# Kernel tuning notes

Hardware: AMD Instinct MI355X
Metric: run time of the kernel (lower is better)

## Reference

```python
import jax, jax.numpy as jnp
import numpy as np

OBS_LEN, K, B, H, MID, NC, CIN = 12, 20, 2048, 128, 256, 2, 3

def setup_inputs() -> dict:
    key = jax.random.key(0)
    ks = jax.random.split(key, 12)
    w = lambda k, s: 0.1 * jax.random.normal(k, s, dtype=jnp.float32)
    return {
        'obs_traj_rel': jax.random.normal(ks[0], (OBS_LEN, B, CIN), dtype=jnp.float32),
        'pred_lstm_hidden': jax.random.normal(ks[1], (K, B, H), dtype=jnp.float32),
        'map_w0': w(ks[2], (H, MID)), 'map_b0': jnp.zeros((MID,), jnp.float32),
        'map_w1': w(ks[3], (MID, H)), 'map_b1': jnp.zeros((H,), jnp.float32),
        'w_ih': w(ks[4], (4 * H, NC)), 'w_hh': w(ks[5], (4 * H, H)),
        'b_ih': jnp.zeros((4 * H,), jnp.float32), 'b_hh': jnp.zeros((4 * H,), jnp.float32),
        'out_w': w(ks[6], (H, NC)), 'out_b': jnp.zeros((NC,), jnp.float32),
    }

def _hard_sigmoid(x):
    # torch F.hardsigmoid: clip(x/6 + 0.5, 0, 1)
    return jnp.clip(x / 6.0 + 0.5, 0.0, 1.0)

def reference(obs_traj_rel, pred_lstm_hidden, map_w0, map_b0, map_w1, map_b1,
              w_ih, w_hh, b_ih, b_hh, out_w, out_b):
    n_coord = out_w.shape[1]
    hdim = w_hh.shape[1]
    # mapping MLP on initial hidden state: [K, B, H]
    h = jax.nn.leaky_relu(pred_lstm_hidden @ map_w0 + map_b0, negative_slope=0.01)
    h = h @ map_w1 + map_b1
    c = jnp.zeros_like(h)
    # step i uses obs[i-1] (obs[0] at i=0), sliced to first n_coord channels
    inputs = jnp.concatenate([obs_traj_rel[:1], obs_traj_rel[:-1]], axis=0)[:, :, :n_coord]  # [T, B, nc]
    bias = b_ih + b_hh

    def step(carry, x_t):
        h, c = carry  # each [K, B, H]
        # x_t [B, nc] broadcast over samples K (same gates contribution for all K)
        gx = x_t @ w_ih.T  # [B, 4H]
        gates = gx[None, :, :] + h @ w_hh.T + bias  # [K, B, 4H]
        i, f, g, o = jnp.split(gates, 4, axis=-1)
        i = _hard_sigmoid(i); f = _hard_sigmoid(f)
        g = jnp.clip(g, -1.0, 1.0); o = _hard_sigmoid(o)
        c_new = f * c + i * g
        h_new = o * jnp.clip(c_new, -1.0, 1.0)
        out = h_new @ out_w + out_b  # [K, B, nc]
        return (h_new, c_new), out

    _, outs = jax.lax.scan(step, (h, c), inputs)
    return outs  # [obs_len, K, B, n_coord]
```

## Files before the change

### kernel.cpp

```cpp
#include <hip/hip_runtime.h>
#include <stdint.h>

#define OBS_LEN 12
#define KS 20
#define BB 2048
#define HD 128
#define MIDD 256
#define NCQ 2

using f32x4  = __attribute__((ext_vector_type(4))) float;
using bf16x8 = __attribute__((ext_vector_type(8))) short;

static __device__ __forceinline__ short f2bf(float f){
  return __builtin_bit_cast(short, (__bf16)f);
}
static __device__ __forceinline__ uint32_t pack2(float a, float b){
  return (uint32_t)(uint16_t)f2bf(a) | ((uint32_t)(uint16_t)f2bf(b) << 16);
}
static __device__ __forceinline__ float hsig(float x){
  return fminf(fmaxf(fmaf(x, 0.16666666666666666f, 0.5f), 0.f), 1.f);
}
static __device__ __forceinline__ float clip1(float x){
  return fminf(fmaxf(x, -1.f), 1.f);
}
static __device__ __forceinline__ f32x4 mm(bf16x8 a, bf16x8 b, f32x4 c){
  return __builtin_amdgcn_mfma_f32_16x16x32_bf16(a, b, c, 0, 0, 0);
}
static __device__ __forceinline__ bf16x8 ldh(const uint16_t* buf, int row, int q, int p){
  return *reinterpret_cast<const bf16x8*>(&buf[(row*HD + q*32 + p*8) ^ ((row&7)*8)]);
}
static __device__ __forceinline__ bf16x8 lda(const uint16_t* buf, int row, int q, int p){
  return *reinterpret_cast<const bf16x8*>(&buf[(row*MIDD + q*32 + p*8) ^ ((row&7)*8)]);
}

__global__ __launch_bounds__(512, 2)
void CRMF_35296041239144_kernel(
    const float* __restrict__ obs,  const float* __restrict__ pred,
    const float* __restrict__ mw0,  const float* __restrict__ mb0,
    const float* __restrict__ mw1,  const float* __restrict__ mb1,
    const float* __restrict__ wih,  const float* __restrict__ whh,
    const float* __restrict__ bih,  const float* __restrict__ bhh,
    const float* __restrict__ oww,  const float* __restrict__ obb,
    float* __restrict__ outp)
{
  __shared__ __align__(16) uint16_t hbuf[32*HD];
  __shared__ __align__(16) uint16_t abuf[32*MIDD];
  __shared__ __align__(16) uint16_t ofrag[4*64*8];
  __shared__ float2 xbuf[OBS_LEN][32];

  const int tid = threadIdx.x;
  const int w   = tid >> 6;
  const int l   = tid & 63;
  const int p   = (tid >> 4) & 3;
  const int ln  = tid & 15;
  const int wofs = w * 16;
  const bool w7 = (w == 7);

  const int b     = blockIdx.x;
  const int b0    = (b & 63) * 32;
  const int kslot = b >> 6;

  if (tid < OBS_LEN*32){
    int t = tid >> 5, cc = tid & 31;
    int st = t ? (t-1) : 0;
    const float* pp = obs + ((size_t)st*BB + b0 + cc)*3;
    xbuf[t][cc] = make_float2(pp[0], pp[1]);
  }
  if (w == 0){
    #pragma unroll
    for (int q=0; q<4; ++q){
      bf16x8 wf;
      #pragma unroll
      for (int j=0; j<8; ++j){
        int k = q*32 + p*8 + j;
        wf[j] = (ln < NCQ) ? f2bf(oww[k*NCQ + ln]) : (short)0;
      }
      *reinterpret_cast<bf16x8*>(&ofrag[(q*64 + l)*8]) = wf;
    }
  }
  const float obv = (ln < NCQ) ? obb[ln] : 0.f;

  bf16x8 wfrag[4][4];
  float wihA[4], wihB[4], biasv[4];
  #pragma unroll
  for (int gate=0; gate<4; ++gate){
    int col = gate*128 + wofs + ln;
    wihA[gate]  = wih[col*2];
    wihB[gate]  = wih[col*2+1];
    biasv[gate] = bih[col] + bhh[col];
    #pragma unroll
    for (int q=0; q<4; ++q){
      const float* s = whh + col*HD + q*32 + p*8;
      float4 f0 = *reinterpret_cast<const float4*>(s);
      float4 f1 = *reinterpret_cast<const float4*>(s+4);
      bf16x8 wf;
      wf[0]=f2bf(f0.x); wf[1]=f2bf(f0.y); wf[2]=f2bf(f0.z); wf[3]=f2bf(f0.w);
      wf[4]=f2bf(f1.x); wf[5]=f2bf(f1.y); wf[6]=f2bf(f1.z); wf[7]=f2bf(f1.w);
      wfrag[gate][q] = wf;
    }
  }

  #pragma unroll 1
  for (int c=0; c<5; ++c){
    const int kk = kslot*5 + c;

    __syncthreads();
    {
      const float* src = pred + ((size_t)(kk*BB + b0))*HD;
      #pragma unroll
      for (int it=0; it<2; ++it){
        int u = tid + it*512;
        int row = u >> 5, c4 = (u & 31)*4;
        float4 v = *reinterpret_cast<const float4*>(src + row*HD + c4);
        int e = (row*HD + c4) ^ ((row&7)*8);
        *reinterpret_cast<uint32_t*>(&hbuf[e])   = pack2(v.x, v.y);
        *reinterpret_cast<uint32_t*>(&hbuf[e+2]) = pack2(v.z, v.w);
      }
    }
    __syncthreads();

    {
      f32x4 acc1[2][2];
      #pragma unroll
      for (int ct=0; ct<2; ++ct){
        float mb = mb0[w*32 + ct*16 + ln];
        f32x4 v = {mb,mb,mb,mb};
        acc1[0][ct]=v; acc1[1][ct]=v;
      }
      #pragma unroll
      for (int q=0; q<4; ++q){
        bf16x8 af0 = ldh(hbuf, ln, q, p), af1 = ldh(hbuf, 16+ln, q, p);
        #pragma unroll
        for (int ct=0; ct<2; ++ct){
          bf16x8 wf;
          #pragma unroll
          for (int j=0; j<8; ++j)
            wf[j] = f2bf(mw0[(q*32+p*8+j)*MIDD + (w*32 + ct*16 + ln)]);
          acc1[0][ct] = mm(af0, wf, acc1[0][ct]);
          acc1[1][ct] = mm(af1, wf, acc1[1][ct]);
        }
      }
      #pragma unroll
      for (int rt=0; rt<2; ++rt)
      #pragma unroll
      for (int ct=0; ct<2; ++ct)
      #pragma unroll
      for (int r=0; r<4; ++r){
        float v = acc1[rt][ct][r];
        v = (v>0.f)? v : 0.01f*v;
        int row = rt*16 + p*4 + r;
        abuf[(row*MIDD + w*32 + ct*16 + ln) ^ ((row&7)*8)] = (uint16_t)f2bf(v);
      }
    }
    __syncthreads();

    float c_[2][4];
    {
      f32x4 acc2[2];
      float mb = mb1[wofs + ln];
      f32x4 v = {mb,mb,mb,mb};
      acc2[0]=v; acc2[1]=v;
      #pragma unroll
      for (int q=0; q<8; ++q){
        bf16x8 af0 = lda(abuf, ln, q, p), af1 = lda(abuf, 16+ln, q, p);
        bf16x8 wf;
        #pragma unroll
        for (int j=0; j<8; ++j)
          wf[j] = f2bf(mw1[(q*32+p*8+j)*HD + wofs + ln]);
        acc2[0] = mm(af0, wf, acc2[0]);
        acc2[1] = mm(af1, wf, acc2[1]);
      }
      #pragma unroll
      for (int rt=0; rt<2; ++rt)
      #pragma unroll
      for (int r=0; r<4; ++r){
        int row = rt*16 + p*4 + r;
        hbuf[(row*HD + wofs + ln) ^ ((row&7)*8)] = (uint16_t)f2bf(acc2[rt][r]);
        c_[rt][r] = 0.f;
      }
    }
    __syncthreads();

    #pragma unroll 1
    for (int t=0; t<OBS_LEN; ++t){
      f32x4 acc[2][4];
      #pragma unroll
      for (int rt=0; rt<2; ++rt){
        #pragma unroll
        for (int r=0; r<4; ++r){
          float2 xv = xbuf[t][rt*16 + p*4 + r];
          #pragma unroll
          for (int gate=0; gate<4; ++gate)
            acc[rt][gate][r] = fmaf(xv.x, wihA[gate], fmaf(xv.y, wihB[gate], biasv[gate]));
        }
      }
      f32x4 a8[2];
      if (w7 && t>0){ f32x4 v={obv,obv,obv,obv}; a8[0]=v; a8[1]=v; }
      #pragma unroll
      for (int q=0; q<4; ++q){
        bf16x8 af0 = ldh(hbuf, ln, q, p), af1 = ldh(hbuf, 16+ln, q, p);
        #pragma unroll
        for (int gate=0; gate<4; ++gate){
          acc[0][gate] = mm(af0, wfrag[gate][q], acc[0][gate]);
          acc[1][gate] = mm(af1, wfrag[gate][q], acc[1][gate]);
        }
        if (w7 && t>0){
          bf16x8 of = *reinterpret_cast<const bf16x8*>(&ofrag[(q*64 + l)*8]);
          a8[0] = mm(af0, of, a8[0]);
          a8[1] = mm(af1, of, a8[1]);
        }
      }
      if (w7 && t>0 && ln<NCQ){
        #pragma unroll
        for (int rt=0; rt<2; ++rt)
        #pragma unroll
        for (int r=0; r<4; ++r){
          int cell = rt*16 + p*4 + r;
          outp[(((size_t)(t-1)*KS + kk)*BB + b0 + cell)*NCQ + ln] = a8[rt][r];
        }
      }
      __syncthreads();
      #pragma unroll
      for (int rt=0; rt<2; ++rt)
      #pragma unroll
      for (int r=0; r<4; ++r){
        float iv = hsig(acc[rt][0][r]);
        float fv = hsig(acc[rt][1][r]);
        float gv = clip1(acc[rt][2][r]);
        float ov = hsig(acc[rt][3][r]);
        float cv = fmaf(fv, c_[rt][r], iv*gv);
        c_[rt][r] = cv;
        int row = rt*16 + p*4 + r;
        hbuf[(row*HD + wofs + ln) ^ ((row&7)*8)] = (uint16_t)f2bf(ov * clip1(cv));
      }
      __syncthreads();
    }

    if (w7){
      f32x4 o0 = {obv,obv,obv,obv}, o1 = o0;
      #pragma unroll
      for (int q=0; q<4; ++q){
        bf16x8 af0 = ldh(hbuf, ln, q, p), af1 = ldh(hbuf, 16+ln, q, p);
        bf16x8 of = *reinterpret_cast<const bf16x8*>(&ofrag[(q*64 + l)*8]);
        o0 = mm(af0, of, o0);
        o1 = mm(af1, of, o1);
      }
      if (ln < NCQ){
        #pragma unroll
        for (int r=0; r<4; ++r){
          outp[(((size_t)11*KS + kk)*BB + b0 +      (p*4+r))*NCQ + ln] = o0[r];
          outp[(((size_t)11*KS + kk)*BB + b0 + 16 + (p*4+r))*NCQ + ln] = o1[r];
        }
      }
    }
  }
}

extern "C" void kernel_launch(void* const* d_in, const int* in_sizes, int n_in,
                              void* d_out, int out_size, void* d_ws, size_t ws_size,
                              hipStream_t stream) {
  (void)in_sizes; (void)n_in; (void)d_ws; (void)ws_size; (void)out_size;
  CRMF_35296041239144_kernel<<<dim3(256), dim3(512), 0, stream>>>(
      (const float*)d_in[0], (const float*)d_in[1], (const float*)d_in[2],
      (const float*)d_in[3], (const float*)d_in[4], (const float*)d_in[5],
      (const float*)d_in[6], (const float*)d_in[7], (const float*)d_in[8],
      (const float*)d_in[9], (const float*)d_in[10], (const float*)d_in[11],
      (float*)d_out);
}
```

Measured before the change: 171.2 us.

## Split K across more blocks, double-buffer hidden state, stage output stores

The grid doubles to 512 blocks. Each block now handles 3 or 2 interleaved sample chunks instead of 5, which shortens the per-block serial path and fills more of the GPU. The LSTM hidden state is double-buffered in LDS, which removes one __syncthreads per timestep. Per-step output writes from a single wave are staged in LDS and flushed with coalesced stores once per chunk. The cost is uneven work across blocks (3 chunks versus 2) and extra shared memory, which may limit co-residency.

```diff
diff --git a/kernel.cpp b/kernel.cpp
--- a/kernel.cpp
+++ b/kernel.cpp
@@ -43,10 +43,11 @@
     const float* __restrict__ oww,  const float* __restrict__ obb,
     float* __restrict__ outp)
 {
-  __shared__ __align__(16) uint16_t hbuf[32*HD];
+  __shared__ __align__(16) uint16_t hbuf[2][32*HD];
   __shared__ __align__(16) uint16_t abuf[32*MIDD];
   __shared__ __align__(16) uint16_t ofrag[4*64*8];
   __shared__ float2 xbuf[OBS_LEN][32];
+  __shared__ float  ostage[OBS_LEN][64];
 
   const int tid = threadIdx.x;
   const int w   = tid >> 6;
@@ -56,9 +57,9 @@
   const int wofs = w * 16;
   const bool w7 = (w == 7);
 
-  const int b     = blockIdx.x;
-  const int b0    = (b & 63) * 32;
-  const int kslot = b >> 6;
+  const int b   = blockIdx.x;
+  const int b0  = (b & 63) * 32;
+  const int nch = (b < 256) ? 3 : 2;
 
   if (tid < OBS_LEN*32){
     int t = tid >> 5, cc = tid & 31;
@@ -101,8 +102,8 @@
   }
 
   #pragma unroll 1
-  for (int c=0; c<5; ++c){
-    const int kk = kslot*5 + c;
+  for (int i=0; i<nch; ++i){
+    const int kk = (b >> 6) + 8*i;
 
     __syncthreads();
     {
@@ -113,8 +114,8 @@
         int row = u >> 5, c4 = (u & 31)*4;
         float4 v = *reinterpret_cast<const float4*>(src + row*HD + c4);
         int e = (row*HD + c4) ^ ((row&7)*8);
-        *reinterpret_cast<uint32_t*>(&hbuf[e])   = pack2(v.x, v.y);
-        *reinterpret_cast<uint32_t*>(&hbuf[e+2]) = pack2(v.z, v.w);
+        *reinterpret_cast<uint32_t*>(&hbuf[0][e])   = pack2(v.x, v.y);
+        *reinterpret_cast<uint32_t*>(&hbuf[0][e+2]) = pack2(v.z, v.w);
       }
     }
     __syncthreads();
@@ -129,7 +130,7 @@
       }
       #pragma unroll
       for (int q=0; q<4; ++q){
-        bf16x8 af0 = ldh(hbuf, ln, q, p), af1 = ldh(hbuf, 16+ln, q, p);
+        bf16x8 af0 = ldh(hbuf[0], ln, q, p), af1 = ldh(hbuf[0], 16+ln, q, p);
         #pragma unroll
         for (int ct=0; ct<2; ++ct){
           bf16x8 wf;
@@ -175,7 +176,7 @@
       #pragma unroll
       for (int r=0; r<4; ++r){
         int row = rt*16 + p*4 + r;
-        hbuf[(row*HD + wofs + ln) ^ ((row&7)*8)] = (uint16_t)f2bf(acc2[rt][r]);
+        hbuf[0][(row*HD + wofs + ln) ^ ((row&7)*8)] = (uint16_t)f2bf(acc2[rt][r]);
         c_[rt][r] = 0.f;
       }
     }
@@ -183,6 +184,7 @@
 
     #pragma unroll 1
     for (int t=0; t<OBS_LEN; ++t){
+      const int cur = t & 1, nxt = cur ^ 1;
       f32x4 acc[2][4];
       #pragma unroll
       for (int rt=0; rt<2; ++rt){
@@ -198,7 +200,7 @@
       if (w7 && t>0){ f32x4 v={obv,obv,obv,obv}; a8[0]=v; a8[1]=v; }
       #pragma unroll
       for (int q=0; q<4; ++q){
-        bf16x8 af0 = ldh(hbuf, ln, q, p), af1 = ldh(hbuf, 16+ln, q, p);
+        bf16x8 af0 = ldh(hbuf[cur], ln, q, p), af1 = ldh(hbuf[cur], 16+ln, q, p);
         #pragma unroll
         for (int gate=0; gate<4; ++gate){
           acc[0][gate] = mm(af0, wfrag[gate][q], acc[0][gate]);
@@ -214,12 +216,9 @@
         #pragma unroll
         for (int rt=0; rt<2; ++rt)
         #pragma unroll
-        for (int r=0; r<4; ++r){
-          int cell = rt*16 + p*4 + r;
-          outp[(((size_t)(t-1)*KS + kk)*BB + b0 + cell)*NCQ + ln] = a8[rt][r];
-        }
-      }
-      __syncthreads();
+        for (int r=0; r<4; ++r)
+          ostage[t-1][(rt*16 + p*4 + r)*NCQ + ln] = a8[rt][r];
+      }
       #pragma unroll
       for (int rt=0; rt<2; ++rt)
       #pragma unroll
@@ -231,7 +230,7 @@
         float cv = fmaf(fv, c_[rt][r], iv*gv);
         c_[rt][r] = cv;
         int row = rt*16 + p*4 + r;
-        hbuf[(row*HD + wofs + ln) ^ ((row&7)*8)] = (uint16_t)f2bf(ov * clip1(cv));
+        hbuf[nxt][(row*HD + wofs + ln) ^ ((row&7)*8)] = (uint16_t)f2bf(ov * clip1(cv));
       }
       __syncthreads();
     }
@@ -240,7 +239,7 @@
       f32x4 o0 = {obv,obv,obv,obv}, o1 = o0;
       #pragma unroll
       for (int q=0; q<4; ++q){
-        bf16x8 af0 = ldh(hbuf, ln, q, p), af1 = ldh(hbuf, 16+ln, q, p);
+        bf16x8 af0 = ldh(hbuf[0], ln, q, p), af1 = ldh(hbuf[0], 16+ln, q, p);
         bf16x8 of = *reinterpret_cast<const bf16x8*>(&ofrag[(q*64 + l)*8]);
         o0 = mm(af0, of, o0);
         o1 = mm(af1, of, o1);
@@ -248,10 +247,16 @@
       if (ln < NCQ){
         #pragma unroll
         for (int r=0; r<4; ++r){
-          outp[(((size_t)11*KS + kk)*BB + b0 +      (p*4+r))*NCQ + ln] = o0[r];
-          outp[(((size_t)11*KS + kk)*BB + b0 + 16 + (p*4+r))*NCQ + ln] = o1[r];
-        }
-      }
+          ostage[11][(     p*4 + r)*NCQ + ln] = o0[r];
+          ostage[11][(16 + p*4 + r)*NCQ + ln] = o1[r];
+        }
+      }
+    }
+    __syncthreads();
+
+    for (int u = tid; u < OBS_LEN*64; u += 512){
+      int t = u >> 6, e = u & 63;
+      outp[((size_t)(t*KS + kk)*BB + b0)*NCQ + e] = ostage[t][e];
     }
   }
 }
@@ -260,7 +265,7 @@
                               void* d_out, int out_size, void* d_ws, size_t ws_size,
                               hipStream_t stream) {
   (void)in_sizes; (void)n_in; (void)d_ws; (void)ws_size; (void)out_size;
-  CRMF_35296041239144_kernel<<<dim3(256), dim3(512), 0, stream>>>(
+  CRMF_35296041239144_kernel<<<dim3(512), dim3(512), 0, stream>>>(
       (const float*)d_in[0], (const float*)d_in[1], (const float*)d_in[2],
       (const float*)d_in[3], (const float*)d_in[4], (const float*)d_in[5],
       (const float*)d_in[6], (const float*)d_in[7], (const float*)d_in[8],
```

After: 213.0 us. 24.4% more time.

## Interleave two K-samples per block, double-buffer hidden state, prepack bf16 weights

Applied to the files above, without the earlier changes.

Each block now runs two sample slices (kk pairs) at once through the mapping MLP and LSTM recurrence. This doubles the independent MFMA chains per wave, which hides MFMA latency and halves the number of barrier-separated steps. The hidden state is double-buffered in shared memory, so one __syncthreads per timestep replaces two. A separate prep kernel converts and pre-swizzles W_hh, the mapping weights and the output weights into bf16 fragment layout in the workspace, replacing per-element strided fp32 loads and conversions. The cost is roughly double the LDS footprint and more registers, which may cut occupancy below the two blocks per CU the launch bounds request, plus one extra kernel launch.

```diff
diff --git a/kernel.cpp b/kernel.cpp
--- a/kernel.cpp
+++ b/kernel.cpp
@@ -8,6 +8,12 @@
 #define MIDD 256
 #define NCQ 2
 
+#define WSW_OFF  0
+#define WSM0_OFF 65536
+#define WSM1_OFF 98304
+#define WSO_OFF  131072
+#define WS_ELEMS 133120
+
 using f32x4  = __attribute__((ext_vector_type(4))) float;
 using bf16x8 = __attribute__((ext_vector_type(8))) short;
 
@@ -33,6 +39,299 @@
   return *reinterpret_cast<const bf16x8*>(&buf[(row*MIDD + q*32 + p*8) ^ ((row&7)*8)]);
 }
 
+__global__ void CRMF_prep_kernel(const float* __restrict__ mw0,
+                                 const float* __restrict__ mw1,
+                                 const float* __restrict__ whh,
+                                 const float* __restrict__ oww,
+                                 uint16_t* __restrict__ ws)
+{
+  int f = blockIdx.x*256 + threadIdx.x;
+  if (f >= 16640) return;
+  bf16x8 out;
+  int dst;
+  if (f < 8192){
+    int l=f&63, q=(f>>6)&3, gate=(f>>8)&3, w=f>>10;
+    int col = gate*128 + w*16 + (l&15);
+    const float* s = whh + col*HD + q*32 + ((l>>4)&3)*8;
+    #pragma unroll
+    for (int j=0;j<8;++j) out[j] = f2bf(s[j]);
+    dst = WSW_OFF + f*8;
+  } else if (f < 12288){
+    int ff=f-8192; int l=ff&63, q=(ff>>6)&3, ct=(ff>>8)&1, w=ff>>9;
+    int col = w*32 + ct*16 + (l&15);
+    int r0 = q*32 + ((l>>4)&3)*8;
+    #pragma unroll
+    for (int j=0;j<8;++j) out[j] = f2bf(mw0[(r0+j)*MIDD + col]);
+    dst = WSM0_OFF + ff*8;
+  } else if (f < 16384){
+    int ff=f-12288; int l=ff&63, q=(ff>>6)&7, w=ff>>9;
+    int col = w*16 + (l&15);
+    int r0 = q*32 + ((l>>4)&3)*8;
+    #pragma unroll
+    for (int j=0;j<8;++j) out[j] = f2bf(mw1[(r0+j)*HD + col]);
+    dst = WSM1_OFF + ff*8;
+  } else {
+    int ff=f-16384; int l=ff&63, q=ff>>6;
+    int ln=l&15; int r0 = q*32 + ((l>>4)&3)*8;
+    #pragma unroll
+    for (int j=0;j<8;++j) out[j] = (ln<NCQ) ? f2bf(oww[(r0+j)*NCQ + ln]) : (short)0;
+    dst = WSO_OFF + ff*8;
+  }
+  *reinterpret_cast<bf16x8*>(&ws[dst]) = out;
+}
+
+template<bool FWS, bool HASB>
+static __device__ __forceinline__ void run_pair(
+    int kkA, int kkB, int b0,
+    const float* __restrict__ pred,
+    const float* __restrict__ mb0, const float* __restrict__ mb1,
+    const float* __restrict__ mw0, const float* __restrict__ mw1,
+    const uint16_t* __restrict__ ws,
+    const bf16x8 (&wfrag)[4][4],
+    const float (&wihA)[4], const float (&wihB)[4], const float (&biasv)[4],
+    const uint16_t* ofrag, float obv,
+    uint16_t (*hA)[32*HD], uint16_t (*hB)[32*HD],
+    uint16_t* abA, uint16_t* abB,
+    const float2 (&xbuf)[OBS_LEN][32],
+    float* __restrict__ outp,
+    int tid, int w, int l, int p, int ln, int wofs, bool w7)
+{
+  __syncthreads();
+
+  {
+    const float* srcA = pred + ((size_t)(kkA*BB + b0))*HD;
+    #pragma unroll
+    for (int it=0; it<2; ++it){
+      int u = tid + it*512;
+      int row = u >> 5, c4 = (u & 31)*4;
+      float4 v = *reinterpret_cast<const float4*>(srcA + row*HD + c4);
+      int e = (row*HD + c4) ^ ((row&7)*8);
+      *reinterpret_cast<uint32_t*>(&hA[0][e])   = pack2(v.x, v.y);
+      *reinterpret_cast<uint32_t*>(&hA[0][e+2]) = pack2(v.z, v.w);
+    }
+    if constexpr (HASB){
+      const float* srcB = pred + ((size_t)(kkB*BB + b0))*HD;
+      #pragma unroll
+      for (int it=0; it<2; ++it){
+        int u = tid + it*512;
+        int row = u >> 5, c4 = (u & 31)*4;
+        float4 v = *reinterpret_cast<const float4*>(srcB + row*HD + c4);
+        int e = (row*HD + c4) ^ ((row&7)*8);
+        *reinterpret_cast<uint32_t*>(&hB[0][e])   = pack2(v.x, v.y);
+        *reinterpret_cast<uint32_t*>(&hB[0][e+2]) = pack2(v.z, v.w);
+      }
+    }
+  }
+  __syncthreads();
+
+  {
+    f32x4 a1A[2][2], a1B[2][2];
+    #pragma unroll
+    for (int ct=0; ct<2; ++ct){
+      float mb = mb0[w*32 + ct*16 + ln];
+      f32x4 v = {mb,mb,mb,mb};
+      a1A[0][ct]=v; a1A[1][ct]=v;
+      if constexpr (HASB){ a1B[0][ct]=v; a1B[1][ct]=v; }
+    }
+    #pragma unroll
+    for (int q=0; q<4; ++q){
+      bf16x8 aA0 = ldh(hA[0], ln, q, p), aA1 = ldh(hA[0], 16+ln, q, p);
+      bf16x8 aB0, aB1;
+      if constexpr (HASB){ aB0 = ldh(hB[0], ln, q, p); aB1 = ldh(hB[0], 16+ln, q, p); }
+      #pragma unroll
+      for (int ct=0; ct<2; ++ct){
+        bf16x8 wf;
+        if constexpr (FWS){
+          wf = *reinterpret_cast<const bf16x8*>(&ws[WSM0_OFF + (((w*2+ct)*4+q)*64 + l)*8]);
+        } else {
+          #pragma unroll
+          for (int j=0; j<8; ++j)
+            wf[j] = f2bf(mw0[(q*32+p*8+j)*MIDD + (w*32 + ct*16 + ln)]);
+        }
+        a1A[0][ct] = mm(aA0, wf, a1A[0][ct]);
+        a1A[1][ct] = mm(aA1, wf, a1A[1][ct]);
+        if constexpr (HASB){
+          a1B[0][ct] = mm(aB0, wf, a1B[0][ct]);
+          a1B[1][ct] = mm(aB1, wf, a1B[1][ct]);
+        }
+      }
+    }
+    #pragma unroll
+    for (int rt=0; rt<2; ++rt)
+    #pragma unroll
+    for (int ct=0; ct<2; ++ct)
+    #pragma unroll
+    for (int r=0; r<4; ++r){
+      int row = rt*16 + p*4 + r;
+      int e = (row*MIDD + w*32 + ct*16 + ln) ^ ((row&7)*8);
+      float vA = a1A[rt][ct][r];
+      abA[e] = (uint16_t)f2bf(vA>0.f ? vA : 0.01f*vA);
+      if constexpr (HASB){
+        float vB = a1B[rt][ct][r];
+        abB[e] = (uint16_t)f2bf(vB>0.f ? vB : 0.01f*vB);
+      }
+    }
+  }
+  __syncthreads();
+
+  float cA[2][4], cB[2][4];
+  {
+    f32x4 a2A[2], a2B[2];
+    float mb = mb1[wofs + ln];
+    f32x4 v = {mb,mb,mb,mb};
+    a2A[0]=v; a2A[1]=v;
+    if constexpr (HASB){ a2B[0]=v; a2B[1]=v; }
+    #pragma unroll
+    for (int q=0; q<8; ++q){
+      bf16x8 aA0 = lda(abA, ln, q, p), aA1 = lda(abA, 16+ln, q, p);
+      bf16x8 aB0, aB1;
+      if constexpr (HASB){ aB0 = lda(abB, ln, q, p); aB1 = lda(abB, 16+ln, q, p); }
+      bf16x8 wf;
+      if constexpr (FWS){
+        wf = *reinterpret_cast<const bf16x8*>(&ws[WSM1_OFF + ((w*8+q)*64 + l)*8]);
+      } else {
+        #pragma unroll
+        for (int j=0; j<8; ++j)
+          wf[j] = f2bf(mw1[(q*32+p*8+j)*HD + wofs + ln]);
+      }
+      a2A[0] = mm(aA0, wf, a2A[0]);
+      a2A[1] = mm(aA1, wf, a2A[1]);
+      if constexpr (HASB){
+        a2B[0] = mm(aB0, wf, a2B[0]);
+        a2B[1] = mm(aB1, wf, a2B[1]);
+      }
+    }
+    #pragma unroll
+    for (int rt=0; rt<2; ++rt)
+    #pragma unroll
+    for (int r=0; r<4; ++r){
+      int row = rt*16 + p*4 + r;
+      int e = (row*HD + wofs + ln) ^ ((row&7)*8);
+      hA[0][e] = (uint16_t)f2bf(a2A[rt][r]);
+      cA[rt][r] = 0.f;
+      if constexpr (HASB){
+        hB[0][e] = (uint16_t)f2bf(a2B[rt][r]);
+        cB[rt][r] = 0.f;
+      }
+    }
+  }
+  __syncthreads();
+
+  #pragma unroll 1
+  for (int t=0; t<OBS_LEN; ++t){
+    const int cur = t & 1, nxt = cur ^ 1;
+    f32x4 accA[2][4], accB[2][4];
+    #pragma unroll
+    for (int rt=0; rt<2; ++rt){
+      #pragma unroll
+      for (int r=0; r<4; ++r){
+        float2 xv = xbuf[t][rt*16 + p*4 + r];
+        #pragma unroll
+        for (int gate=0; gate<4; ++gate){
+          float a = fmaf(xv.x, wihA[gate], fmaf(xv.y, wihB[gate], biasv[gate]));
+          accA[rt][gate][r] = a;
+          if constexpr (HASB) accB[rt][gate][r] = a;
+        }
+      }
+    }
+    f32x4 a8A[2], a8B[2];
+    if (w7 && t>0){
+      f32x4 v={obv,obv,obv,obv};
+      a8A[0]=v; a8A[1]=v;
+      if constexpr (HASB){ a8B[0]=v; a8B[1]=v; }
+    }
+    #pragma unroll
+    for (int q=0; q<4; ++q){
+      bf16x8 aA0 = ldh(hA[cur], ln, q, p), aA1 = ldh(hA[cur], 16+ln, q, p);
+      bf16x8 aB0, aB1;
+      if constexpr (HASB){ aB0 = ldh(hB[cur], ln, q, p); aB1 = ldh(hB[cur], 16+ln, q, p); }
+      #pragma unroll
+      for (int gate=0; gate<4; ++gate){
+        accA[0][gate] = mm(aA0, wfrag[gate][q], accA[0][gate]);
+        accA[1][gate] = mm(aA1, wfrag[gate][q], accA[1][gate]);
+        if constexpr (HASB){
+          accB[0][gate] = mm(aB0, wfrag[gate][q], accB[0][gate]);
+          accB[1][gate] = mm(aB1, wfrag[gate][q], accB[1][gate]);
+        }
+      }
+      if (w7 && t>0){
+        bf16x8 of = *reinterpret_cast<const bf16x8*>(&ofrag[(q*64 + l)*8]);
+        a8A[0] = mm(aA0, of, a8A[0]);
+        a8A[1] = mm(aA1, of, a8A[1]);
+        if constexpr (HASB){
+          a8B[0] = mm(aB0, of, a8B[0]);
+          a8B[1] = mm(aB1, of, a8B[1]);
+        }
+      }
+    }
+    if (w7 && t>0 && ln<NCQ){
+      #pragma unroll
+      for (int rt=0; rt<2; ++rt)
+      #pragma unroll
+      for (int r=0; r<4; ++r){
+        int cell = rt*16 + p*4 + r;
+        outp[(((size_t)(t-1)*KS + kkA)*BB + b0 + cell)*NCQ + ln] = a8A[rt][r];
+        if constexpr (HASB)
+          outp[(((size_t)(t-1)*KS + kkB)*BB + b0 + cell)*NCQ + ln] = a8B[rt][r];
+      }
+    }
+    #pragma unroll
+    for (int rt=0; rt<2; ++rt)
+    #pragma unroll
+    for (int r=0; r<4; ++r){
+      int row = rt*16 + p*4 + r;
+      int e = (row*HD + wofs + ln) ^ ((row&7)*8);
+      {
+        float iv = hsig(accA[rt][0][r]);
+        float fv = hsig(accA[rt][1][r]);
+        float gv = clip1(accA[rt][2][r]);
+        float ov = hsig(accA[rt][3][r]);
+        float cv = fmaf(fv, cA[rt][r], iv*gv);
+        cA[rt][r] = cv;
+        hA[nxt][e] = (uint16_t)f2bf(ov * clip1(cv));
+      }
+      if constexpr (HASB){
+        float iv = hsig(accB[rt][0][r]);
+        float fv = hsig(accB[rt][1][r]);
+        float gv = clip1(accB[rt][2][r]);
+        float ov = hsig(accB[rt][3][r]);
+        float cv = fmaf(fv, cB[rt][r], iv*gv);
+        cB[rt][r] = cv;
+        hB[nxt][e] = (uint16_t)f2bf(ov * clip1(cv));
+      }
+    }
+    __syncthreads();
+  }
+
+  if (w7){
+    f32x4 oA0 = {obv,obv,obv,obv}, oA1 = oA0, oB0 = oA0, oB1 = oA0;
+    #pragma unroll
+    for (int q=0; q<4; ++q){
+      bf16x8 of = *reinterpret_cast<const bf16x8*>(&ofrag[(q*64 + l)*8]);
+      bf16x8 aA0 = ldh(hA[0], ln, q, p), aA1 = ldh(hA[0], 16+ln, q, p);
+      oA0 = mm(aA0, of, oA0);
+      oA1 = mm(aA1, of, oA1);
+      if constexpr (HASB){
+        bf16x8 aB0 = ldh(hB[0], ln, q, p), aB1 = ldh(hB[0], 16+ln, q, p);
+        oB0 = mm(aB0, of, oB0);
+        oB1 = mm(aB1, of, oB1);
+      }
+    }
+    if (ln < NCQ){
+      #pragma unroll
+      for (int r=0; r<4; ++r){
+        outp[(((size_t)11*KS + kkA)*BB + b0 +      (p*4+r))*NCQ + ln] = oA0[r];
+        outp[(((size_t)11*KS + kkA)*BB + b0 + 16 + (p*4+r))*NCQ + ln] = oA1[r];
+        if constexpr (HASB){
+          outp[(((size_t)11*KS + kkB)*BB + b0 +      (p*4+r))*NCQ + ln] = oB0[r];
+          outp[(((size_t)11*KS + kkB)*BB + b0 + 16 + (p*4+r))*NCQ + ln] = oB1[r];
+        }
+      }
+    }
+  }
+}
+
+template<bool FWS>
 __global__ __launch_bounds__(512, 2)
 void CRMF_35296041239144_kernel(
     const float* __restrict__ obs,  const float* __restrict__ pred,
@@ -41,10 +340,13 @@
     const float* __restrict__ wih,  const float* __restrict__ whh,
     const float* __restrict__ bih,  const float* __restrict__ bhh,
     const float* __restrict__ oww,  const float* __restrict__ obb,
+    const uint16_t* __restrict__ ws,
     float* __restrict__ outp)
 {
-  __shared__ __align__(16) uint16_t hbuf[32*HD];
-  __shared__ __align__(16) uint16_t abuf[32*MIDD];
+  __shared__ __align__(16) uint16_t hbufA[2][32*HD];
+  __shared__ __align__(16) uint16_t hbufB[2][32*HD];
+  __shared__ __align__(16) uint16_t abufA[32*MIDD];
+  __shared__ __align__(16) uint16_t abufB[32*MIDD];
   __shared__ __align__(16) uint16_t ofrag[4*64*8];
   __shared__ float2 xbuf[OBS_LEN][32];
 
@@ -66,21 +368,42 @@
     const float* pp = obs + ((size_t)st*BB + b0 + cc)*3;
     xbuf[t][cc] = make_float2(pp[0], pp[1]);
   }
-  if (w == 0){
+  if (tid < 256){
+    if constexpr (FWS){
+      *reinterpret_cast<bf16x8*>(&ofrag[tid*8]) =
+          *reinterpret_cast<const bf16x8*>(&ws[WSO_OFF + tid*8]);
+    } else {
+      int q = tid >> 6, ll = tid & 63;
+      int lln = ll & 15, pp2 = (ll >> 4) & 3;
+      bf16x8 wf;
+      #pragma unroll
+      for (int j=0; j<8; ++j)
+        wf[j] = (lln < NCQ) ? f2bf(oww[(q*32+pp2*8+j)*NCQ + lln]) : (short)0;
+      *reinterpret_cast<bf16x8*>(&ofrag[tid*8]) = wf;
+    }
+  }
+  const float obv = (ln < NCQ) ? obb[ln] : 0.f;
+
+  bf16x8 wfrag[4][4];
+  #pragma unroll
+  for (int gate=0; gate<4; ++gate){
     #pragma unroll
     for (int q=0; q<4; ++q){
-      bf16x8 wf;
-      #pragma unroll
-      for (int j=0; j<8; ++j){
-        int k = q*32 + p*8 + j;
-        wf[j] = (ln < NCQ) ? f2bf(oww[k*NCQ + ln]) : (short)0;
-      }
-      *reinterpret_cast<bf16x8*>(&ofrag[(q*64 + l)*8]) = wf;
-    }
-  }
-  const float obv = (ln < NCQ) ? obb[ln] : 0.f;
-
-  bf16x8 wfrag[4][4];
+      if constexpr (FWS){
+        wfrag[gate][q] = *reinterpret_cast<const bf16x8*>(
+            &ws[WSW_OFF + (((w*4+gate)*4+q)*64 + l)*8]);
+      } else {
+        int col = gate*128 + wofs + ln;
+        const float* s = whh + col*HD + q*32 + p*8;
+        float4 f0 = *reinterpret_cast<const float4*>(s);
+        float4 f1 = *reinterpret_cast<const float4*>(s+4);
+        bf16x8 wf;
+        wf[0]=f2bf(f0.x); wf[1]=f2bf(f0.y); wf[2]=f2bf(f0.z); wf[3]=f2bf(f0.w);
+        wf[4]=f2bf(f1.x); wf[5]=f2bf(f1.y); wf[6]=f2bf(f1.z); wf[7]=f2bf(f1.w);
+        wfrag[gate][q] = wf;
+      }
+    }
+  }
   float wihA[4], wihB[4], biasv[4];
   #pragma unroll
   for (int gate=0; gate<4; ++gate){
@@ -88,182 +411,49 @@
     wihA[gate]  = wih[col*2];
     wihB[gate]  = wih[col*2+1];
     biasv[gate] = bih[col] + bhh[col];
-    #pragma unroll
-    for (int q=0; q<4; ++q){
-      const float* s = whh + col*HD + q*32 + p*8;
-      float4 f0 = *reinterpret_cast<const float4*>(s);
-      float4 f1 = *reinterpret_cast<const float4*>(s+4);
-      bf16x8 wf;
-      wf[0]=f2bf(f0.x); wf[1]=f2bf(f0.y); wf[2]=f2bf(f0.z); wf[3]=f2bf(f0.w);
-      wf[4]=f2bf(f1.x); wf[5]=f2bf(f1.y); wf[6]=f2bf(f1.z); wf[7]=f2bf(f1.w);
-      wfrag[gate][q] = wf;
-    }
-  }
-
-  #pragma unroll 1
-  for (int c=0; c<5; ++c){
-    const int kk = kslot*5 + c;
-
-    __syncthreads();
-    {
-      const float* src = pred + ((size_t)(kk*BB + b0))*HD;
-      #pragma unroll
-      for (int it=0; it<2; ++it){
-        int u = tid + it*512;
-        int row = u >> 5, c4 = (u & 31)*4;
-        float4 v = *reinterpret_cast<const float4*>(src + row*HD + c4);
-        int e = (row*HD + c4) ^ ((row&7)*8);
-        *reinterpret_cast<uint32_t*>(&hbuf[e])   = pack2(v.x, v.y);
-        *reinterpret_cast<uint32_t*>(&hbuf[e+2]) = pack2(v.z, v.w);
-      }
-    }
-    __syncthreads();
-
-    {
-      f32x4 acc1[2][2];
-      #pragma unroll
-      for (int ct=0; ct<2; ++ct){
-        float mb = mb0[w*32 + ct*16 + ln];
-        f32x4 v = {mb,mb,mb,mb};
-        acc1[0][ct]=v; acc1[1][ct]=v;
-      }
-      #pragma unroll
-      for (int q=0; q<4; ++q){
-        bf16x8 af0 = ldh(hbuf, ln, q, p), af1 = ldh(hbuf, 16+ln, q, p);
-        #pragma unroll
-        for (int ct=0; ct<2; ++ct){
-          bf16x8 wf;
-          #pragma unroll
-          for (int j=0; j<8; ++j)
-            wf[j] = f2bf(mw0[(q*32+p*8+j)*MIDD + (w*32 + ct*16 + ln)]);
-          acc1[0][ct] = mm(af0, wf, acc1[0][ct]);
-          acc1[1][ct] = mm(af1, wf, acc1[1][ct]);
-        }
-      }
-      #pragma unroll
-      for (int rt=0; rt<2; ++rt)
-      #pragma unroll
-      for (int ct=0; ct<2; ++ct)
-      #pragma unroll
-      for (int r=0; r<4; ++r){
-        float v = acc1[rt][ct][r];
-        v = (v>0.f)? v : 0.01f*v;
-        int row = rt*16 + p*4 + r;
-        abuf[(row*MIDD + w*32 + ct*16 + ln) ^ ((row&7)*8)] = (uint16_t)f2bf(v);
-      }
-    }
-    __syncthreads();
-
-    float c_[2][4];
-    {
-      f32x4 acc2[2];
-      float mb = mb1[wofs + ln];
-      f32x4 v = {mb,mb,mb,mb};
-      acc2[0]=v; acc2[1]=v;
-      #pragma unroll
-      for (int q=0; q<8; ++q){
-        bf16x8 af0 = lda(abuf, ln, q, p), af1 = lda(abuf, 16+ln, q, p);
-        bf16x8 wf;
-        #pragma unroll
-        for (int j=0; j<8; ++j)
-          wf[j] = f2bf(mw1[(q*32+p*8+j)*HD + wofs + ln]);
-        acc2[0] = mm(af0, wf, acc2[0]);
-        acc2[1] = mm(af1, wf, acc2[1]);
-      }
-      #pragma unroll
-      for (int rt=0; rt<2; ++rt)
-      #pragma unroll
-      for (int r=0; r<4; ++r){
-        int row = rt*16 + p*4 + r;
-        hbuf[(row*HD + wofs + ln) ^ ((row&7)*8)] = (uint16_t)f2bf(acc2[rt][r]);
-        c_[rt][r] = 0.f;
-      }
-    }
-    __syncthreads();
-
-    #pragma unroll 1
-    for (int t=0; t<OBS_LEN; ++t){
-      f32x4 acc[2][4];
-      #pragma unroll
-      for (int rt=0; rt<2; ++rt){
-        #pragma unroll
-        for (int r=0; r<4; ++r){
-          float2 xv = xbuf[t][rt*16 + p*4 + r];
-          #pragma unroll
-          for (int gate=0; gate<4; ++gate)
-            acc[rt][gate][r] = fmaf(xv.x, wihA[gate], fmaf(xv.y, wihB[gate], biasv[gate]));
-        }
-      }
-      f32x4 a8[2];
-      if (w7 && t>0){ f32x4 v={obv,obv,obv,obv}; a8[0]=v; a8[1]=v; }
-      #pragma unroll
-      for (int q=0; q<4; ++q){
-        bf16x8 af0 = ldh(hbuf, ln, q, p), af1 = ldh(hbuf, 16+ln, q, p);
-        #pragma unroll
-        for (int gate=0; gate<4; ++gate){
-          acc[0][gate] = mm(af0, wfrag[gate][q], acc[0][gate]);
-          acc[1][gate] = mm(af1, wfrag[gate][q], acc[1][gate]);
-        }
-        if (w7 && t>0){
-          bf16x8 of = *reinterpret_cast<const bf16x8*>(&ofrag[(q*64 + l)*8]);
-          a8[0] = mm(af0, of, a8[0]);
-          a8[1] = mm(af1, of, a8[1]);
-        }
-      }
-      if (w7 && t>0 && ln<NCQ){
-        #pragma unroll
-        for (int rt=0; rt<2; ++rt)
-        #pragma unroll
-        for (int r=0; r<4; ++r){
-          int cell = rt*16 + p*4 + r;
-          outp[(((size_t)(t-1)*KS + kk)*BB + b0 + cell)*NCQ + ln] = a8[rt][r];
-        }
-      }
-      __syncthreads();
-      #pragma unroll
-      for (int rt=0; rt<2; ++rt)
-      #pragma unroll
-      for (int r=0; r<4; ++r){
-        float iv = hsig(acc[rt][0][r]);
-        float fv = hsig(acc[rt][1][r]);
-        float gv = clip1(acc[rt][2][r]);
-        float ov = hsig(acc[rt][3][r]);
-        float cv = fmaf(fv, c_[rt][r], iv*gv);
-        c_[rt][r] = cv;
-        int row = rt*16 + p*4 + r;
-        hbuf[(row*HD + wofs + ln) ^ ((row&7)*8)] = (uint16_t)f2bf(ov * clip1(cv));
-      }
-      __syncthreads();
-    }
-
-    if (w7){
-      f32x4 o0 = {obv,obv,obv,obv}, o1 = o0;
-      #pragma unroll
-      for (int q=0; q<4; ++q){
-        bf16x8 af0 = ldh(hbuf, ln, q, p), af1 = ldh(hbuf, 16+ln, q, p);
-        bf16x8 of = *reinterpret_cast<const bf16x8*>(&ofrag[(q*64 + l)*8]);
-        o0 = mm(af0, of, o0);
-        o1 = mm(af1, of, o1);
-      }
-      if (ln < NCQ){
-        #pragma unroll
-        for (int r=0; r<4; ++r){
-          outp[(((size_t)11*KS + kk)*BB + b0 +      (p*4+r))*NCQ + ln] = o0[r];
-          outp[(((size_t)11*KS + kk)*BB + b0 + 16 + (p*4+r))*NCQ + ln] = o1[r];
-        }
-      }
-    }
-  }
+  }
+
+  run_pair<FWS,true >(kslot*5+0, kslot*5+1, b0, pred, mb0, mb1, mw0, mw1, ws,
+                      wfrag, wihA, wihB, biasv, ofrag, obv,
+                      hbufA, hbufB, abufA, abufB, xbuf, outp,
+                      tid, w, l, p, ln, wofs, w7);
+  run_pair<FWS,true >(kslot*5+2, kslot*5+3, b0, pred, mb0, mb1, mw0, mw1, ws,
+                      wfrag, wihA, wihB, biasv, ofrag, obv,
+                      hbufA, hbufB, abufA, abufB, xbuf, outp,
+                      tid, w, l, p, ln, wofs, w7);
+  run_pair<FWS,false>(kslot*5+4, kslot*5+4, b0, pred, mb0, mb1, mw0, mw1, ws,
+                      wfrag, wihA, wihB, biasv, ofrag, obv,
+                      hbufA, hbufB, abufA, abufB, xbuf, outp,
+                      tid, w, l, p, ln, wofs, w7);
 }
 
 extern "C" void kernel_launch(void* const* d_in, const int* in_sizes, int n_in,
                               void* d_out, int out_size, void* d_ws, size_t ws_size,
                               hipStream_t stream) {
-  (void)in_sizes; (void)n_in; (void)d_ws; (void)ws_size; (void)out_size;
-  CRMF_35296041239144_kernel<<<dim3(256), dim3(512), 0, stream>>>(
-      (const float*)d_in[0], (const float*)d_in[1], (const float*)d_in[2],
-      (const float*)d_in[3], (const float*)d_in[4], (const float*)d_in[5],
-      (const float*)d_in[6], (const float*)d_in[7], (const float*)d_in[8],
-      (const float*)d_in[9], (const float*)d_in[10], (const float*)d_in[11],
-      (float*)d_out);
-}
+  (void)in_sizes; (void)n_in; (void)out_size;
+  const float* obs  = (const float*)d_in[0];
+  const float* pred = (const float*)d_in[1];
+  const float* mw0  = (const float*)d_in[2];
+  const float* mb0  = (const float*)d_in[3];
+  const float* mw1  = (const float*)d_in[4];
+  const float* mb1  = (const float*)d_in[5];
+  const float* wih  = (const float*)d_in[6];
+  const float* whh  = (const float*)d_in[7];
+  const float* bih  = (const float*)d_in[8];
+  const float* bhh  = (const float*)d_in[9];
+  const float* oww  = (const float*)d_in[10];
+  const float* obb  = (const float*)d_in[11];
+  float* outp = (float*)d_out;
+
+  if (ws_size >= (size_t)WS_ELEMS * sizeof(uint16_t)){
+    uint16_t* ws = (uint16_t*)d_ws;
+    CRMF_prep_kernel<<<dim3(65), dim3(256), 0, stream>>>(mw0, mw1, whh, oww, ws);
+    CRMF_35296041239144_kernel<true><<<dim3(256), dim3(512), 0, stream>>>(
+        obs, pred, mw0, mb0, mw1, mb1, wih, whh, bih, bhh, oww, obb,
+        (const uint16_t*)ws, outp);
+  } else {
+    CRMF_35296041239144_kernel<false><<<dim3(256), dim3(512), 0, stream>>>(
+        obs, pred, mw0, mb0, mw1, mb1, wih, whh, bih, bhh, oww, obb,
+        (const uint16_t*)nullptr, outp);
+  }
+}
```

Result: slower. 285.1 us (+66.6%).

## Run two K samples per block concurrently with shared W_hh fragments in LDS

Applied to the files above, without the earlier changes.

Each block doubles to 1024 threads split into two 512-thread groups. The groups process different K samples at once, so the per-block loop drops from five sequential samples to three iterations; in the last one both groups redundantly compute the same sample. The recurrent W_hh fragments move out of per-thread registers into a 128KB LDS buffer that both groups share, and the MLP scratch buffer is aliased onto that region. A new prep kernel converts the weights once per call into MFMA-ready bf16 fragment layouts in the workspace, replacing repeated strided fp32 loads and conversions. The trade-off is extra LDS traffic for the weights on every timestep, near-full LDS usage at one block per CU, and duplicated work and writes for the fifth sample.

```diff
diff --git a/kernel.cpp b/kernel.cpp
--- a/kernel.cpp
+++ b/kernel.cpp
@@ -8,6 +8,12 @@
 #define MIDD 256
 #define NCQ 2
 
+#define WSW_OFF  0
+#define WSM0_OFF 65536
+#define WSM1_OFF 98304
+#define WSO_OFF  131072
+#define WS_ELEMS 133120
+
 using f32x4  = __attribute__((ext_vector_type(4))) float;
 using bf16x8 = __attribute__((ext_vector_type(8))) short;
 
@@ -33,7 +39,49 @@
   return *reinterpret_cast<const bf16x8*>(&buf[(row*MIDD + q*32 + p*8) ^ ((row&7)*8)]);
 }
 
-__global__ __launch_bounds__(512, 2)
+__global__ void CRMF_prep_kernel(const float* __restrict__ mw0,
+                                 const float* __restrict__ mw1,
+                                 const float* __restrict__ whh,
+                                 const float* __restrict__ oww,
+                                 uint16_t* __restrict__ ws)
+{
+  int f = blockIdx.x*256 + threadIdx.x;
+  if (f >= 16640) return;
+  bf16x8 out;
+  int dst;
+  if (f < 8192){
+    int l=f&63, q=(f>>6)&3, gate=(f>>8)&3, w=f>>10;
+    int col = gate*128 + w*16 + (l&15);
+    const float* s = whh + col*HD + q*32 + ((l>>4)&3)*8;
+    #pragma unroll
+    for (int j=0;j<8;++j) out[j] = f2bf(s[j]);
+    dst = WSW_OFF + f*8;
+  } else if (f < 12288){
+    int ff=f-8192; int l=ff&63, q=(ff>>6)&3, ct=(ff>>8)&1, w=ff>>9;
+    int col = w*32 + ct*16 + (l&15);
+    int r0 = q*32 + ((l>>4)&3)*8;
+    #pragma unroll
+    for (int j=0;j<8;++j) out[j] = f2bf(mw0[(r0+j)*MIDD + col]);
+    dst = WSM0_OFF + ff*8;
+  } else if (f < 16384){
+    int ff=f-12288; int l=ff&63, q=(ff>>6)&7, w=ff>>9;
+    int col = w*16 + (l&15);
+    int r0 = q*32 + ((l>>4)&3)*8;
+    #pragma unroll
+    for (int j=0;j<8;++j) out[j] = f2bf(mw1[(r0+j)*HD + col]);
+    dst = WSM1_OFF + ff*8;
+  } else {
+    int ff=f-16384; int l=ff&63, q=ff>>6;
+    int ln=l&15; int r0 = q*32 + ((l>>4)&3)*8;
+    #pragma unroll
+    for (int j=0;j<8;++j) out[j] = (ln<NCQ) ? f2bf(oww[(r0+j)*NCQ + ln]) : (short)0;
+    dst = WSO_OFF + ff*8;
+  }
+  *reinterpret_cast<bf16x8*>(&ws[dst]) = out;
+}
+
+template<bool FWS>
+__global__ __launch_bounds__(1024, 1)
 void CRMF_35296041239144_kernel(
     const float* __restrict__ obs,  const float* __restrict__ pred,
     const float* __restrict__ mw0,  const float* __restrict__ mb0,
@@ -41,20 +89,23 @@
     const float* __restrict__ wih,  const float* __restrict__ whh,
     const float* __restrict__ bih,  const float* __restrict__ bhh,
     const float* __restrict__ oww,  const float* __restrict__ obb,
+    const uint16_t* __restrict__ ws,
     float* __restrict__ outp)
 {
-  __shared__ __align__(16) uint16_t hbuf[32*HD];
-  __shared__ __align__(16) uint16_t abuf[32*MIDD];
+  __shared__ __align__(16) uint16_t wlds[65536];
+  __shared__ __align__(16) uint16_t hb[2][32*HD];
   __shared__ __align__(16) uint16_t ofrag[4*64*8];
   __shared__ float2 xbuf[OBS_LEN][32];
 
   const int tid = threadIdx.x;
-  const int w   = tid >> 6;
+  const int g   = tid >> 9;
+  const int lt  = tid & 511;
+  const int cw  = (tid >> 6) & 7;
   const int l   = tid & 63;
   const int p   = (tid >> 4) & 3;
   const int ln  = tid & 15;
-  const int wofs = w * 16;
-  const bool w7 = (w == 7);
+  const int wofs = cw * 16;
+  const bool wOut = (cw == 7);
 
   const int b     = blockIdx.x;
   const int b0    = (b & 63) * 32;
@@ -66,21 +117,22 @@
     const float* pp = obs + ((size_t)st*BB + b0 + cc)*3;
     xbuf[t][cc] = make_float2(pp[0], pp[1]);
   }
-  if (w == 0){
-    #pragma unroll
-    for (int q=0; q<4; ++q){
+  if (tid < 256){
+    if constexpr (FWS){
+      *reinterpret_cast<bf16x8*>(&ofrag[tid*8]) =
+          *reinterpret_cast<const bf16x8*>(&ws[WSO_OFF + tid*8]);
+    } else {
+      int q = tid >> 6, ll = tid & 63;
+      int lln = ll & 15, pp2 = (ll >> 4) & 3;
       bf16x8 wf;
       #pragma unroll
-      for (int j=0; j<8; ++j){
-        int k = q*32 + p*8 + j;
-        wf[j] = (ln < NCQ) ? f2bf(oww[k*NCQ + ln]) : (short)0;
-      }
-      *reinterpret_cast<bf16x8*>(&ofrag[(q*64 + l)*8]) = wf;
+      for (int j=0; j<8; ++j)
+        wf[j] = (lln < NCQ) ? f2bf(oww[(q*32+pp2*8+j)*NCQ + lln]) : (short)0;
+      *reinterpret_cast<bf16x8*>(&ofrag[tid*8]) = wf;
     }
   }
   const float obv = (ln < NCQ) ? obb[ln] : 0.f;
 
-  bf16x8 wfrag[4][4];
   float wihA[4], wihB[4], biasv[4];
   #pragma unroll
   for (int gate=0; gate<4; ++gate){
@@ -88,33 +140,26 @@
     wihA[gate]  = wih[col*2];
     wihB[gate]  = wih[col*2+1];
     biasv[gate] = bih[col] + bhh[col];
-    #pragma unroll
-    for (int q=0; q<4; ++q){
-      const float* s = whh + col*HD + q*32 + p*8;
-      float4 f0 = *reinterpret_cast<const float4*>(s);
-      float4 f1 = *reinterpret_cast<const float4*>(s+4);
-      bf16x8 wf;
-      wf[0]=f2bf(f0.x); wf[1]=f2bf(f0.y); wf[2]=f2bf(f0.z); wf[3]=f2bf(f0.w);
-      wf[4]=f2bf(f1.x); wf[5]=f2bf(f1.y); wf[6]=f2bf(f1.z); wf[7]=f2bf(f1.w);
-      wfrag[gate][q] = wf;
-    }
-  }
+  }
+
+  uint16_t* ab = wlds + g*8192;
 
   #pragma unroll 1
-  for (int c=0; c<5; ++c){
-    const int kk = kslot*5 + c;
-
-    __syncthreads();
+  for (int iter=0; iter<3; ++iter){
+    const int kk = kslot*5 + ((iter<2) ? iter*2 + g : 4);
+
+    __syncthreads();
+
     {
       const float* src = pred + ((size_t)(kk*BB + b0))*HD;
       #pragma unroll
       for (int it=0; it<2; ++it){
-        int u = tid + it*512;
+        int u = lt + it*512;
         int row = u >> 5, c4 = (u & 31)*4;
         float4 v = *reinterpret_cast<const float4*>(src + row*HD + c4);
         int e = (row*HD + c4) ^ ((row&7)*8);
-        *reinterpret_cast<uint32_t*>(&hbuf[e])   = pack2(v.x, v.y);
-        *reinterpret_cast<uint32_t*>(&hbuf[e+2]) = pack2(v.z, v.w);
+        *reinterpret_cast<uint32_t*>(&hb[g][e])   = pack2(v.x, v.y);
+        *reinterpret_cast<uint32_t*>(&hb[g][e+2]) = pack2(v.z, v.w);
       }
     }
     __syncthreads();
@@ -123,19 +168,23 @@
       f32x4 acc1[2][2];
       #pragma unroll
       for (int ct=0; ct<2; ++ct){
-        float mb = mb0[w*32 + ct*16 + ln];
+        float mb = mb0[cw*32 + ct*16 + ln];
         f32x4 v = {mb,mb,mb,mb};
         acc1[0][ct]=v; acc1[1][ct]=v;
       }
       #pragma unroll
       for (int q=0; q<4; ++q){
-        bf16x8 af0 = ldh(hbuf, ln, q, p), af1 = ldh(hbuf, 16+ln, q, p);
+        bf16x8 af0 = ldh(hb[g], ln, q, p), af1 = ldh(hb[g], 16+ln, q, p);
         #pragma unroll
         for (int ct=0; ct<2; ++ct){
           bf16x8 wf;
-          #pragma unroll
-          for (int j=0; j<8; ++j)
-            wf[j] = f2bf(mw0[(q*32+p*8+j)*MIDD + (w*32 + ct*16 + ln)]);
+          if constexpr (FWS){
+            wf = *reinterpret_cast<const bf16x8*>(&ws[WSM0_OFF + (((cw*2+ct)*4+q)*64 + l)*8]);
+          } else {
+            #pragma unroll
+            for (int j=0; j<8; ++j)
+              wf[j] = f2bf(mw0[(q*32+p*8+j)*MIDD + (cw*32 + ct*16 + ln)]);
+          }
           acc1[0][ct] = mm(af0, wf, acc1[0][ct]);
           acc1[1][ct] = mm(af1, wf, acc1[1][ct]);
         }
@@ -149,7 +198,7 @@
         float v = acc1[rt][ct][r];
         v = (v>0.f)? v : 0.01f*v;
         int row = rt*16 + p*4 + r;
-        abuf[(row*MIDD + w*32 + ct*16 + ln) ^ ((row&7)*8)] = (uint16_t)f2bf(v);
+        ab[(row*MIDD + cw*32 + ct*16 + ln) ^ ((row&7)*8)] = (uint16_t)f2bf(v);
       }
     }
     __syncthreads();
@@ -162,11 +211,15 @@
       acc2[0]=v; acc2[1]=v;
       #pragma unroll
       for (int q=0; q<8; ++q){
-        bf16x8 af0 = lda(abuf, ln, q, p), af1 = lda(abuf, 16+ln, q, p);
+        bf16x8 af0 = lda(ab, ln, q, p), af1 = lda(ab, 16+ln, q, p);
         bf16x8 wf;
-        #pragma unroll
-        for (int j=0; j<8; ++j)
-          wf[j] = f2bf(mw1[(q*32+p*8+j)*HD + wofs + ln]);
+        if constexpr (FWS){
+          wf = *reinterpret_cast<const bf16x8*>(&ws[WSM1_OFF + ((cw*8+q)*64 + l)*8]);
+        } else {
+          #pragma unroll
+          for (int j=0; j<8; ++j)
+            wf[j] = f2bf(mw1[(q*32+p*8+j)*HD + wofs + ln]);
+        }
         acc2[0] = mm(af0, wf, acc2[0]);
         acc2[1] = mm(af1, wf, acc2[1]);
       }
@@ -175,8 +228,30 @@
       #pragma unroll
       for (int r=0; r<4; ++r){
         int row = rt*16 + p*4 + r;
-        hbuf[(row*HD + wofs + ln) ^ ((row&7)*8)] = (uint16_t)f2bf(acc2[rt][r]);
+        hb[g][(row*HD + wofs + ln) ^ ((row&7)*8)] = (uint16_t)f2bf(acc2[rt][r]);
         c_[rt][r] = 0.f;
+      }
+    }
+    __syncthreads();
+
+    if constexpr (FWS){
+      #pragma unroll
+      for (int it=0; it<8; ++it){
+        int idx = (tid + it*1024)*8;
+        *reinterpret_cast<bf16x8*>(&wlds[idx]) =
+            *reinterpret_cast<const bf16x8*>(&ws[WSW_OFF + idx]);
+      }
+    } else {
+      #pragma unroll
+      for (int it=0; it<8; ++it){
+        int s = tid + it*1024;
+        int sl=s&63, sq=(s>>6)&3, sg=(s>>8)&3, sw=s>>10;
+        int col = sg*128 + sw*16 + (sl&15);
+        const float* sp = whh + col*HD + sq*32 + ((sl>>4)&3)*8;
+        bf16x8 wf;
+        #pragma unroll
+        for (int j=0;j<8;++j) wf[j] = f2bf(sp[j]);
+        *reinterpret_cast<bf16x8*>(&wlds[s*8]) = wf;
       }
     }
     __syncthreads();
@@ -195,22 +270,24 @@
         }
       }
       f32x4 a8[2];
-      if (w7 && t>0){ f32x4 v={obv,obv,obv,obv}; a8[0]=v; a8[1]=v; }
+      if (wOut && t>0){ f32x4 v={obv,obv,obv,obv}; a8[0]=v; a8[1]=v; }
       #pragma unroll
       for (int q=0; q<4; ++q){
-        bf16x8 af0 = ldh(hbuf, ln, q, p), af1 = ldh(hbuf, 16+ln, q, p);
+        bf16x8 af0 = ldh(hb[g], ln, q, p), af1 = ldh(hb[g], 16+ln, q, p);
         #pragma unroll
         for (int gate=0; gate<4; ++gate){
-          acc[0][gate] = mm(af0, wfrag[gate][q], acc[0][gate]);
-          acc[1][gate] = mm(af1, wfrag[gate][q], acc[1][gate]);
-        }
-        if (w7 && t>0){
+          bf16x8 wf = *reinterpret_cast<const bf16x8*>(
+              &wlds[(((cw*4+gate)*4+q)*64 + l)*8]);
+          acc[0][gate] = mm(af0, wf, acc[0][gate]);
+          acc[1][gate] = mm(af1, wf, acc[1][gate]);
+        }
+        if (wOut && t>0){
           bf16x8 of = *reinterpret_cast<const bf16x8*>(&ofrag[(q*64 + l)*8]);
           a8[0] = mm(af0, of, a8[0]);
           a8[1] = mm(af1, of, a8[1]);
         }
       }
-      if (w7 && t>0 && ln<NCQ){
+      if (wOut && t>0 && ln<NCQ){
         #pragma unroll
         for (int rt=0; rt<2; ++rt)
         #pragma unroll
@@ -231,16 +308,16 @@
         float cv = fmaf(fv, c_[rt][r], iv*gv);
         c_[rt][r] = cv;
         int row = rt*16 + p*4 + r;
-        hbuf[(row*HD + wofs + ln) ^ ((row&7)*8)] = (uint16_t)f2bf(ov * clip1(cv));
+        hb[g][(row*HD + wofs + ln) ^ ((row&7)*8)] = (uint16_t)f2bf(ov * clip1(cv));
       }
       __syncthreads();
     }
 
-    if (w7){
+    if (wOut){
       f32x4 o0 = {obv,obv,obv,obv}, o1 = o0;
       #pragma unroll
       for (int q=0; q<4; ++q){
-        bf16x8 af0 = ldh(hbuf, ln, q, p), af1 = ldh(hbuf, 16+ln, q, p);
+        bf16x8 af0 = ldh(hb[g], ln, q, p), af1 = ldh(hb[g], 16+ln, q, p);
         bf16x8 of = *reinterpret_cast<const bf16x8*>(&ofrag[(q*64 + l)*8]);
         o0 = mm(af0, of, o0);
         o1 = mm(af1, of, o1);
@@ -259,11 +336,30 @@
 extern "C" void kernel_launch(void* const* d_in, const int* in_sizes, int n_in,
                               void* d_out, int out_size, void* d_ws, size_t ws_size,
                               hipStream_t stream) {
-  (void)in_sizes; (void)n_in; (void)d_ws; (void)ws_size; (void)out_size;
-  CRMF_35296041239144_kernel<<<dim3(256), dim3(512), 0, stream>>>(
-      (const float*)d_in[0], (const float*)d_in[1], (const float*)d_in[2],
-      (const float*)d_in[3], (const float*)d_in[4], (const float*)d_in[5],
-      (const float*)d_in[6], (const float*)d_in[7], (const float*)d_in[8],
-      (const float*)d_in[9], (const float*)d_in[10], (const float*)d_in[11],
-      (float*)d_out);
-}
+  (void)in_sizes; (void)n_in; (void)out_size;
+  const float* obs  = (const float*)d_in[0];
+  const float* pred = (const float*)d_in[1];
+  const float* mw0  = (const float*)d_in[2];
+  const float* mb0  = (const float*)d_in[3];
+  const float* mw1  = (const float*)d_in[4];
+  const float* mb1  = (const float*)d_in[5];
+  const float* wih  = (const float*)d_in[6];
+  const float* whh  = (const float*)d_in[7];
+  const float* bih  = (const float*)d_in[8];
+  const float* bhh  = (const float*)d_in[9];
+  const float* oww  = (const float*)d_in[10];
+  const float* obb  = (const float*)d_in[11];
+  float* outp = (float*)d_out;
+
+  if (ws_size >= (size_t)WS_ELEMS * sizeof(uint16_t)){
+    uint16_t* ws = (uint16_t*)d_ws;
+    CRMF_prep_kernel<<<dim3(65), dim3(256), 0, stream>>>(mw0, mw1, whh, oww, ws);
+    CRMF_35296041239144_kernel<true><<<dim3(256), dim3(1024), 0, stream>>>(
+        obs, pred, mw0, mb0, mw1, mb1, wih, whh, bih, bhh, oww, obb,
+        (const uint16_t*)ws, outp);
+  } else {
+    CRMF_35296041239144_kernel<false><<<dim3(256), dim3(1024), 0, stream>>>(
+        obs, pred, mw0, mb0, mw1, mb1, wih, whh, bih, bhh, oww, obb,
+        (const uint16_t*)nullptr, outp);
+  }
+}
```

Measured after the change: 284.2 us. 66.0% more time.
